# Kernel tuning notes

Hardware: AMD Instinct MI355X
Metric: run time of the kernel (lower is better)

Reference implementation:

```python
import jax, jax.numpy as jnp
import numpy as np

B, N, ND = 4096, 28, 3        # batch, nodes (2 hands x 14 joints), xyz
ED, DD = 512, 256             # encoder dim, decoder dim
H, DH = 8, 64                 # heads, dim_head (inner = 512)
EDEPTH, DDEPTH = 2, 1
EMLP, DMLP = 4 * ED, 4 * DD
NM = 14                       # num_masked = int(0.5 * 28)


def _ln(x, s, b):
    m = jnp.mean(x, -1, keepdims=True)
    v = jnp.var(x, -1, keepdims=True)
    return (x - m) * jax.lax.rsqrt(v + 1e-5) * s + b


def _transformer(x, a, ln1_s, ln1_b, Wqkv, Wo, bo, ln2_s, ln2_b, W1, b1, W2, b2):
    # pre-norm transformer; adjacency a [b,n,n] enters as an additive attention bias
    b, n, _ = x.shape
    scale = DH ** -0.5
    for i in range(ln1_s.shape[0]):
        h = _ln(x, ln1_s[i], ln1_b[i])
        q, k, v = jnp.split(h @ Wqkv[i], 3, axis=-1)
        q = q.reshape(b, n, H, DH).transpose(0, 2, 1, 3)
        k = k.reshape(b, n, H, DH).transpose(0, 2, 1, 3)
        v = v.reshape(b, n, H, DH).transpose(0, 2, 1, 3)
        dots = jnp.einsum('bhid,bhjd->bhij', q, k) * scale + a[:, None]
        attn = jax.nn.softmax(dots, axis=-1)
        o = jnp.einsum('bhij,bhjd->bhid', attn, v).transpose(0, 2, 1, 3).reshape(b, n, H * DH)
        x = x + o @ Wo[i] + bo[i]
        h2 = _ln(x, ln2_s[i], ln2_b[i])
        x = x + jax.nn.gelu(h2 @ W1[i] + b1[i]) @ W2[i] + b2[i]
    return x


def setup_inputs() -> dict:
    key = jax.random.key(0)
    ks = iter(jax.random.split(key, 40))
    nrm = lambda shp, s=0.02: jax.random.normal(next(ks), shp, dtype=jnp.float32) * s
    x = jax.random.normal(next(ks), (B, N, ND), dtype=jnp.float32)
    a = jax.random.uniform(next(ks), (B, N, N), dtype=jnp.float32)
    perm = jnp.argsort(jax.random.uniform(next(ks), (B, N)), axis=-1).astype(jnp.int32)
    masked_indices, unmasked_indices = perm[:, :NM], perm[:, NM:]
    inp = dict(x=x, a=a, masked_indices=masked_indices, unmasked_indices=unmasked_indices)
    inp.update(
        W_emb=nrm((ND, ED)), b_emb=jnp.zeros((ED,), jnp.float32), pos_emb=nrm((N, ED), 0.02),
        e_ln1_s=jnp.ones((EDEPTH, ED)), e_ln1_b=jnp.zeros((EDEPTH, ED)),
        e_Wqkv=nrm((EDEPTH, ED, 3 * H * DH)), e_Wo=nrm((EDEPTH, H * DH, ED)), e_bo=jnp.zeros((EDEPTH, ED)),
        e_ln2_s=jnp.ones((EDEPTH, ED)), e_ln2_b=jnp.zeros((EDEPTH, ED)),
        e_W1=nrm((EDEPTH, ED, EMLP)), e_b1=jnp.zeros((EDEPTH, EMLP)),
        e_W2=nrm((EDEPTH, EMLP, ED)), e_b2=jnp.zeros((EDEPTH, ED)),
        enc2dec_W=nrm((ED, DD)), enc2dec_b=jnp.zeros((DD,), jnp.float32),
        mask_token=nrm((DD,), 1.0), dec_pos_emb=nrm((N, DD), 0.02),
        d_ln1_s=jnp.ones((DDEPTH, DD)), d_ln1_b=jnp.zeros((DDEPTH, DD)),
        d_Wqkv=nrm((DDEPTH, DD, 3 * H * DH)), d_Wo=nrm((DDEPTH, H * DH, DD)), d_bo=jnp.zeros((DDEPTH, DD)),
        d_ln2_s=jnp.ones((DDEPTH, DD)), d_ln2_b=jnp.zeros((DDEPTH, DD)),
        d_W1=nrm((DDEPTH, DD, DMLP)), d_b1=jnp.zeros((DDEPTH, DMLP)),
        d_W2=nrm((DDEPTH, DMLP, DD)), d_b2=jnp.zeros((DDEPTH, DD)),
        pred_W=nrm((DD, ND)), pred_b=jnp.zeros((ND,), jnp.float32),
    )
    return inp


def reference(x, a, masked_indices, unmasked_indices,
              W_emb, b_emb, pos_emb,
              e_ln1_s, e_ln1_b, e_Wqkv, e_Wo, e_bo, e_ln2_s, e_ln2_b, e_W1, e_b1, e_W2, e_b2,
              enc2dec_W, enc2dec_b, mask_token, dec_pos_emb,
              d_ln1_s, d_ln1_b, d_Wqkv, d_Wo, d_bo, d_ln2_s, d_ln2_b, d_W1, d_b1, d_W2, d_b2,
              pred_W, pred_b):
    # node embedding (1x1 conv over nodes == per-node linear) + positional embedding
    tokens = x @ W_emb + b_emb + pos_emb                                   # [B,N,ED]
    unm_tok = jnp.take_along_axis(tokens, unmasked_indices[:, :, None], axis=1)  # [B,N-NM,ED]
    masked_nodes = jnp.take_along_axis(x, masked_indices[:, :, None], axis=1)    # [B,NM,ND]
    # batched adjacency slicing (replaces the per-sample python loop in torch)
    unmasked_a = jax.vmap(lambda ai, ii: ai[ii[:, None], ii[None, :]])(a, unmasked_indices)
    enc = _transformer(unm_tok, unmasked_a,
                       e_ln1_s, e_ln1_b, e_Wqkv, e_Wo, e_bo, e_ln2_s, e_ln2_b, e_W1, e_b1, e_W2, e_b2)
    dec_tok = enc @ enc2dec_W + enc2dec_b                                  # [B,N-NM,DD]
    mask_toks = mask_token + dec_pos_emb[masked_indices]                   # [B,NM,DD]
    # NOTE: faithful to original: unmasked pos-emb tokens are computed but NOT used in the cat
    decoder_tokens = jnp.concatenate([mask_toks, dec_tok], axis=1)         # [B,N,DD]
    decoded = _transformer(decoder_tokens, a,
                           d_ln1_s, d_ln1_b, d_Wqkv, d_Wo, d_bo, d_ln2_s, d_ln2_b, d_W1, d_b1, d_W2, d_b2)
    mt = jnp.take_along_axis(decoded, masked_indices[:, :, None], axis=1)  # [B,NM,DD]
    masked_pred = mt @ pred_W + pred_b                                     # [B,NM,ND]
    recon_loss = jnp.mean((masked_pred - masked_nodes) ** 2)
    return (decoder_tokens, masked_nodes, masked_indices, masked_pred, recon_loss)
```

## Files before the change

kernel.cpp:

```cpp
#include <hip/hip_runtime.h>
#include <math.h>

#define B_TOT 4096
#define N_SEQ 28
#define NDIM 3
#define ED 512
#define DD 256
#define NH 8
#define DHD 64
#define EMLP 2048
#define DMLP 1024
#define NM 14
#define NU 14

typedef __attribute__((ext_vector_type(8))) short short8;
typedef __attribute__((ext_vector_type(4))) float f32x4;
typedef unsigned short ushort_t;
typedef unsigned int uint_t;

__device__ __forceinline__ float gelu_f(float x) {
    float t = 0.7978845608028654f * (x + 0.044715f * x * x * x);
    float e = __expf(2.0f * t);
    float th = 1.0f - 2.0f / (e + 1.0f);
    return 0.5f * x * (1.0f + th);
}
__device__ __forceinline__ ushort_t f2bf(float f) {
    union { float f; uint_t u; } c; c.f = f;
    uint_t u = c.u;
    return (ushort_t)((u + 0x7FFFu + ((u >> 16) & 1u)) >> 16);
}
__device__ __forceinline__ float bf2f(ushort_t h) {
    union { uint_t u; float f; } c; c.u = ((uint_t)h) << 16;
    return c.f;
}
__device__ __forceinline__ float bf_lo(uint_t u) {
    union { uint_t u; float f; } c; c.u = u << 16;
    return c.f;
}
__device__ __forceinline__ float bf_hi(uint_t u) {
    union { uint_t u; float f; } c; c.u = u & 0xFFFF0000u;
    return c.f;
}
__device__ __forceinline__ void gl_lds16(const ushort_t* g, ushort_t* l) {
    __builtin_amdgcn_global_load_lds(
        (const __attribute__((address_space(1))) unsigned int*)g,
        (__attribute__((address_space(3))) unsigned int*)l, 16, 0, 0);
}

__global__ void k_zero(float* p) { p[threadIdx.x] = 0.0f; }
__global__ void k_final(const float* acc, float* out) {
    out[0] = acc[0] * (1.0f / (float)(B_TOT * NM * NDIM));
}

__global__ void k_wconv(const float* __restrict__ W, ushort_t* __restrict__ Wt, int K, int N) {
    __shared__ float tile[32][33];
    int n0 = blockIdx.x * 32, k0 = blockIdx.y * 32;
    int tr = threadIdx.x >> 5, tc = threadIdx.x & 31;
#pragma unroll
    for (int i = 0; i < 4; ++i)
        tile[tr + i * 8][tc] = W[(size_t)(k0 + tr + i * 8) * N + n0 + tc];
    __syncthreads();
#pragma unroll
    for (int i = 0; i < 4; ++i)
        Wt[(size_t)(n0 + tr + i * 8) * K + k0 + tc] = f2bf(tile[tc][tr + i * 8]);
}

__global__ void k_embed(const float* __restrict__ x, const float* __restrict__ a,
                        const int* __restrict__ mi, const int* __restrict__ ui,
                        const float* __restrict__ W_emb, const float* __restrict__ b_emb,
                        const float* __restrict__ pos_emb,
                        ushort_t* __restrict__ X, float* __restrict__ ua,
                        float* __restrict__ out_mn, float* __restrict__ out_midx,
                        int base) {
    int s = blockIdx.x;
    int g = base + s;
    int t = threadIdx.x;
    for (int i = 0; i < NU; ++i) {
        int u = ui[g * NU + i];
        float x0 = x[((size_t)g * N_SEQ + u) * NDIM + 0];
        float x1 = x[((size_t)g * N_SEQ + u) * NDIM + 1];
        float x2 = x[((size_t)g * N_SEQ + u) * NDIM + 2];
        for (int d = t; d < ED; d += 256) {
            X[((size_t)s * NU + i) * ED + d] = f2bf(
                x0 * W_emb[d] + x1 * W_emb[ED + d] + x2 * W_emb[2 * ED + d]
                + b_emb[d] + pos_emb[(size_t)u * ED + d]);
        }
    }
    for (int idx = t; idx < NU * NU; idx += 256) {
        int i = idx / NU, j = idx % NU;
        int uii = ui[g * NU + i], ujj = ui[g * NU + j];
        ua[(size_t)s * NU * NU + idx] = a[(size_t)g * N_SEQ * N_SEQ + (size_t)uii * N_SEQ + ujj];
    }
    for (int idx = t; idx < NM * NDIM; idx += 256) {
        int i = idx / NDIM, c = idx % NDIM;
        int m = mi[g * NM + i];
        out_mn[((size_t)g * NM + i) * NDIM + c] = x[((size_t)g * N_SEQ + m) * NDIM + c];
    }
    for (int i = t; i < NM; i += 256) {
        out_midx[(size_t)g * NM + i] = (float)mi[g * NM + i];
    }
}

template <int D>
__global__ void k_ln(const ushort_t* __restrict__ in, ushort_t* __restrict__ out,
                     const float* __restrict__ sc, const float* __restrict__ bi, int M) {
    int wave = threadIdx.x >> 6;
    int lane = threadIdx.x & 63;
    int row = blockIdx.x * 4 + wave;
    if (row >= M) return;
    constexpr int PL = D / 64;
    const ushort_t* rp = in + (size_t)row * D + lane * PL;
    uint_t u[PL / 2];
    if (PL == 8) *(uint4*)u = *(const uint4*)rp;
    else *(uint2*)u = *(const uint2*)rp;
    float v[PL];
    float sum = 0.f, sq = 0.f;
#pragma unroll
    for (int q = 0; q < PL / 2; ++q) {
        v[2 * q] = bf_lo(u[q]);
        v[2 * q + 1] = bf_hi(u[q]);
    }
#pragma unroll
    for (int j = 0; j < PL; ++j) { sum += v[j]; sq += v[j] * v[j]; }
#pragma unroll
    for (int o = 32; o >= 1; o >>= 1) {
        sum += __shfl_xor(sum, o);
        sq += __shfl_xor(sq, o);
    }
    float mean = sum * (1.0f / D);
    float var = sq * (1.0f / D) - mean * mean;
    float r = rsqrtf(var + 1e-5f);
    uint_t w[PL / 2];
#pragma unroll
    for (int q = 0; q < PL / 2; ++q) {
        int d = lane * PL + 2 * q;
        float a0 = (v[2 * q] - mean) * r * sc[d] + bi[d];
        float a1 = (v[2 * q + 1] - mean) * r * sc[d + 1] + bi[d + 1];
        w[q] = (uint_t)f2bf(a0) | ((uint_t)f2bf(a1) << 16);
    }
    ushort_t* op = out + (size_t)row * D + lane * PL;
    if (PL == 8) *(uint4*)op = *(uint4*)w;
    else *(uint2*)op = *(uint2*)w;
}

template <int ACT>
__global__ __launch_bounds__(256) void k_gemm_mfma(
    const ushort_t* __restrict__ A, const ushort_t* __restrict__ Wt,
    const float* __restrict__ bias, const ushort_t* __restrict__ res,
    ushort_t* __restrict__ Cout, int M, int N, int K) {
    __shared__ __align__(16) ushort_t smem[17408];
    ushort_t* As0 = smem;
    ushort_t* As1 = smem + 4096;
    ushort_t* Bs0 = smem + 8192;
    ushort_t* Bs1 = smem + 12288;

    const int t = threadIdx.x;
    const int gx = gridDim.x;
    int flat = blockIdx.y * gx + blockIdx.x;
    int nwg = gx * gridDim.y;
    int q8 = nwg >> 3, r8 = nwg & 7;
    int xcd = flat & 7, loc = flat >> 3;
    int wg = (xcd < r8 ? xcd * (q8 + 1) : r8 * (q8 + 1) + (xcd - r8) * q8) + loc;
    const int bm = wg / gx, bn = wg % gx;

    const int lane = t & 63;
    const int wave = t >> 6;
    const int wr = wave >> 1, wc = wave & 1;
    const int l15 = lane & 15;
    const int g4 = lane >> 4;
    const int kg = g4 * 8;

    const int srow = wave * 32 + (lane >> 2);
    const int scol = (lane & 3) * 8;
    const ushort_t* Ag = A + (size_t)(bm * 128 + srow) * K + scol;
    const ushort_t* Bg = Wt + (size_t)(bn * 128 + srow) * K + scol;
    const int wb0 = (wave * 32) * 32;
    const int wb1 = (wave * 32 + 16) * 32;

    f32x4 acc[4][4] = {};
    const int nt = K >> 5;

    gl_lds16(Ag, As0 + wb0);
    gl_lds16(Ag + (size_t)16 * K, As0 + wb1);
    gl_lds16(Bg, Bs0 + wb0);
    gl_lds16(Bg + (size_t)16 * K, Bs0 + wb1);

    for (int tt = 0; tt < nt; ++tt) {
        ushort_t* Ac = (tt & 1) ? As1 : As0;
        ushort_t* Bc = (tt & 1) ? Bs1 : Bs0;
        if (tt + 1 < nt) {
            int k0 = (tt + 1) << 5;
            ushort_t* An = (tt & 1) ? As0 : As1;
            ushort_t* Bn = (tt & 1) ? Bs0 : Bs1;
            gl_lds16(Ag + k0, An + wb0);
            gl_lds16(Ag + (size_t)16 * K + k0, An + wb1);
            gl_lds16(Bg + k0, Bn + wb0);
            gl_lds16(Bg + (size_t)16 * K + k0, Bn + wb1);
            asm volatile("s_waitcnt vmcnt(4)" ::: "memory");
        } else {
            asm volatile("s_waitcnt vmcnt(0)" ::: "memory");
        }
        __builtin_amdgcn_s_barrier();
        __builtin_amdgcn_sched_barrier(0);
        short8 af[4], bfr[4];
#pragma unroll
        for (int m = 0; m < 4; ++m)
            af[m] = *(const short8*)&Ac[(wr * 64 + m * 16 + l15) * 32 + kg];
#pragma unroll
        for (int n = 0; n < 4; ++n)
            bfr[n] = *(const short8*)&Bc[(wc * 64 + n * 16 + l15) * 32 + kg];
#pragma unroll
        for (int m = 0; m < 4; ++m)
#pragma unroll
            for (int n = 0; n < 4; ++n)
                acc[m][n] = __builtin_amdgcn_mfma_f32_16x16x32_bf16(af[m], bfr[n], acc[m][n], 0, 0, 0);
        __builtin_amdgcn_sched_barrier(0);
        __builtin_amdgcn_s_barrier();
    }

    ushort_t* Cs = smem;
    const int erow0 = wr * 64, ecol0 = wc * 64;
#pragma unroll
    for (int m = 0; m < 4; ++m)
#pragma unroll
        for (int n = 0; n < 4; ++n)
#pragma unroll
            for (int r = 0; r < 4; ++r) {
                float v = acc[m][n][r];
                float o = __shfl_xor(v, 1);
                if (!(l15 & 1)) {
                    uint_t pk = (uint_t)f2bf(v) | ((uint_t)f2bf(o) << 16);
                    *(uint_t*)&Cs[(erow0 + m * 16 + g4 * 4 + r) * 136 + ecol0 + n * 16 + l15] = pk;
                }
            }
    __builtin_amdgcn_s_barrier();

    const int row = t >> 1, half = t & 1;
    const int grow = bm * 128 + row;
    const int gc0 = bn * 128 + half * 64;
    const ushort_t* rres = res ? res + (size_t)grow * N + gc0 : (const ushort_t*)0;
    ushort_t* gout = Cout + (size_t)grow * N + gc0;
#pragma unroll
    for (int c = 0; c < 8; ++c) {
        uint4 pv = *(const uint4*)&Cs[row * 136 + half * 64 + c * 8];
        uint_t* pw = (uint_t*)&pv;
        float vv[8];
#pragma unroll
        for (int q = 0; q < 4; ++q) { vv[2 * q] = bf_lo(pw[q]); vv[2 * q + 1] = bf_hi(pw[q]); }
        if (bias) {
#pragma unroll
            for (int j = 0; j < 8; ++j) vv[j] += bias[gc0 + c * 8 + j];
        }
        if (res) {
            uint4 rv = *(const uint4*)(rres + c * 8);
            uint_t* pr = (uint_t*)&rv;
#pragma unroll
            for (int q = 0; q < 4; ++q) { vv[2 * q] += bf_lo(pr[q]); vv[2 * q + 1] += bf_hi(pr[q]); }
        }
        if (ACT == 1) {
#pragma unroll
            for (int j = 0; j < 8; ++j) vv[j] = gelu_f(vv[j]);
        }
        uint4 ov;
        uint_t* po = (uint_t*)&ov;
#pragma unroll
        for (int q = 0; q < 4; ++q)
            po[q] = (uint_t)f2bf(vv[2 * q]) | ((uint_t)f2bf(vv[2 * q + 1]) << 16);
        *(uint4*)(gout + c * 8) = ov;
    }
}

template <int NT>
__global__ __launch_bounds__(256) void k_attn_mfma(
    const ushort_t* __restrict__ qkv, const float* __restrict__ bias,
    ushort_t* __restrict__ O) {
    constexpr int NTP = (NT + 15) & ~15;
    constexpr int MT = NTP / 16;
    constexpr int QS = 72;
    constexpr int VS = 40;
    __shared__ __align__(16) ushort_t smem[4 * NTP * QS * 2 + 4 * 64 * VS];
    ushort_t* Qs = smem;
    ushort_t* Ks = smem + 4 * NTP * QS;
    ushort_t* Vs = Ks + 4 * NTP * QS;
    ushort_t* Ps = smem;

    const int s = blockIdx.x, hg = blockIdx.y;
    const int t = threadIdx.x;
    const int wave = t >> 6, lane = t & 63;
    const int l15 = lane & 15, g4 = lane >> 4;

    const ushort_t* qb = qkv + (size_t)s * NT * 1536 + hg * 256;
    for (int c = t; c < 64 * NT; c += 256) {
        int c8 = c & 7;
        int rem = c >> 3;
        int r = rem % NT;
        int ph = rem / NT;
        int h = ph & 3, p = ph >> 2;
        uint4 v = *(const uint4*)(qb + (size_t)r * 1536 + p * 512 + h * 64 + c8 * 8);
        ushort_t* dst = (p ? Ks : Qs) + (h * NTP + r) * QS + c8 * 8;
        *(uint4*)dst = v;
    }
    const ushort_t* vrow = qkv + (size_t)s * NT * 1536 + 1024 + hg * 256;
    for (int c = t; c < 4 * 64 * (32 - NT); c += 256) {
        int p = c % (32 - NT);
        int hd = c / (32 - NT);
        Vs[hd * VS + NT + p] = 0;
    }
    for (int c = t; c < 4 * NT * 8; c += 256) {
        int c8 = c & 7;
        int r = (c >> 3) % NT;
        int h = (c >> 3) / NT;
        uint4 v = *(const uint4*)(vrow + (size_t)r * 1536 + h * 64 + c8 * 8);
        const uint_t* pv = (const uint_t*)&v;
#pragma unroll
        for (int j = 0; j < 4; ++j) {
            Vs[(h * 64 + c8 * 8 + 2 * j) * VS + r] = (ushort_t)(pv[j] & 0xFFFFu);
            Vs[(h * 64 + c8 * 8 + 2 * j + 1) * VS + r] = (ushort_t)(pv[j] >> 16);
        }
    }
    __syncthreads();

    const int h = wave;
    const ushort_t* Qh = Qs + h * NTP * QS;
    const ushort_t* Kh = Ks + h * NTP * QS;
    const ushort_t* Vh = Vs + h * 64 * VS;
    ushort_t* Ph = Ps + h * NTP * VS;

    f32x4 sacc[MT][MT] = {};
#pragma unroll
    for (int ks = 0; ks < 2; ++ks) {
        short8 qf[MT], kf[MT];
#pragma unroll
        for (int m = 0; m < MT; ++m)
            qf[m] = *(const short8*)&Qh[(m * 16 + l15) * QS + ks * 32 + g4 * 8];
#pragma unroll
        for (int n = 0; n < MT; ++n)
            kf[n] = *(const short8*)&Kh[(n * 16 + l15) * QS + ks * 32 + g4 * 8];
#pragma unroll
        for (int m = 0; m < MT; ++m)
#pragma unroll
            for (int n = 0; n < MT; ++n)
                sacc[m][n] = __builtin_amdgcn_mfma_f32_16x16x32_bf16(qf[m], kf[n], sacc[m][n], 0, 0, 0);
    }

    const float* bp = bias + (size_t)s * NT * NT;
    float prv[MT][MT][4];
#pragma unroll
    for (int m = 0; m < MT; ++m) {
#pragma unroll
        for (int r = 0; r < 4; ++r) {
            int i = m * 16 + g4 * 4 + r;
            float sv[MT];
#pragma unroll
            for (int n = 0; n < MT; ++n) {
                int j = n * 16 + l15;
                sv[n] = (i < NT && j < NT) ? sacc[m][n][r] * 0.125f + bp[i * NT + j] : -1e30f;
            }
            float mx = sv[0];
            if (MT > 1) mx = fmaxf(mx, sv[MT - 1]);
#pragma unroll
            for (int o = 1; o < 16; o <<= 1) mx = fmaxf(mx, __shfl_xor(mx, o));
            float sum = 0.f;
#pragma unroll
            for (int n = 0; n < MT; ++n) {
                float e = (sv[n] > -1e29f) ? __expf(sv[n] - mx) : 0.f;
                prv[m][n][r] = e;
                sum += e;
            }
#pragma unroll
            for (int o = 1; o < 16; o <<= 1) sum += __shfl_xor(sum, o);
            float rs = sum > 0.f ? 1.0f / sum : 0.f;
#pragma unroll
            for (int n = 0; n < MT; ++n) prv[m][n][r] *= rs;
        }
    }
    __syncthreads();

    if (NTP == 16) {
        for (int z = lane; z < 16 * 8; z += 64) {
            int i = z >> 3, jw = z & 7;
            *(uint_t*)&Ph[i * VS + 16 + jw * 2] = 0;
        }
    }
#pragma unroll
    for (int m = 0; m < MT; ++m)
#pragma unroll
        for (int n = 0; n < MT; ++n)
#pragma unroll
            for (int r = 0; r < 4; ++r)
                Ph[(m * 16 + g4 * 4 + r) * VS + n * 16 + l15] = f2bf(prv[m][n][r]);
    __syncthreads();

    f32x4 oacc[MT][4] = {};
    {
        short8 pf[MT], vf[4];
#pragma unroll
        for (int m = 0; m < MT; ++m)
            pf[m] = *(const short8*)&Ph[(m * 16 + l15) * VS + g4 * 8];
#pragma unroll
        for (int nd = 0; nd < 4; ++nd)
            vf[nd] = *(const short8*)&Vh[(nd * 16 + l15) * VS + g4 * 8];
#pragma unroll
        for (int m = 0; m < MT; ++m)
#pragma unroll
            for (int nd = 0; nd < 4; ++nd)
                oacc[m][nd] = __builtin_amdgcn_mfma_f32_16x16x32_bf16(pf[m], vf[nd], oacc[m][nd], 0, 0, 0);
    }

    ushort_t* Ob = O + (size_t)s * NT * 512 + hg * 256 + h * 64;
#pragma unroll
    for (int m = 0; m < MT; ++m)
#pragma unroll
        for (int r = 0; r < 4; ++r) {
            int i = m * 16 + g4 * 4 + r;
            if (i < NT) {
#pragma unroll
                for (int nd = 0; nd < 4; ++nd)
                    Ob[(size_t)i * 512 + nd * 16 + l15] = f2bf(oacc[m][nd][r]);
            }
        }
}

__global__ void k_build_dec(const ushort_t* __restrict__ dec_tok, const float* __restrict__ mask_token,
                            const float* __restrict__ dec_pos, const int* __restrict__ mi,
                            ushort_t* __restrict__ Xd, float* __restrict__ out0, int base) {
    int s = blockIdx.x;
    int g = base + s;
    int t = threadIdx.x;
    for (int idx = t; idx < N_SEQ * DD; idx += 256) {
        int i = idx / DD, d = idx % DD;
        float v;
        if (i < NM) {
            int m = mi[g * NM + i];
            v = mask_token[d] + dec_pos[(size_t)m * DD + d];
        } else {
            v = bf2f(dec_tok[((size_t)s * NU + (i - NM)) * DD + d]);
        }
        Xd[((size_t)s * N_SEQ + i) * DD + d] = f2bf(v);
        out0[((size_t)g * N_SEQ + i) * DD + d] = v;
    }
}

__global__ void k_pred(const ushort_t* __restrict__ Xd, const int* __restrict__ mi,
                       const float* __restrict__ pW, const float* __restrict__ pb,
                       const float* __restrict__ mn, float* __restrict__ out_pred,
                       float* __restrict__ loss, int base, int Bc) {
    int tid = blockIdx.x * 256 + threadIdx.x;
    int total = Bc * NM * NDIM;
    float part = 0.f;
    if (tid < total) {
        int c = tid % NDIM;
        int r = tid / NDIM;
        int i = r % NM;
        int s = r / NM;
        int g = base + s;
        int m = mi[g * NM + i];
        const ushort_t* row = Xd + ((size_t)s * N_SEQ + m) * DD;
        float acc = pb[c];
        for (int k = 0; k < DD; ++k) acc += bf2f(row[k]) * pW[k * NDIM + c];
        out_pred[((size_t)g * NM + i) * NDIM + c] = acc;
        float d = acc - mn[((size_t)g * NM + i) * NDIM + c];
        part = d * d;
    }
    __shared__ float red[256];
    red[threadIdx.x] = part;
    __syncthreads();
    for (int o = 128; o > 0; o >>= 1) {
        if (threadIdx.x < o) red[threadIdx.x] += red[threadIdx.x + o];
        __syncthreads();
    }
    if (threadIdx.x == 0) atomicAdd(loss, red[0]);
}

extern "C" void kernel_launch(void* const* d_in, const int* in_sizes, int n_in,
                              void* d_out, int out_size, void* d_ws, size_t ws_size,
                              hipStream_t stream) {
    const float* x       = (const float*)d_in[0];
    const float* a       = (const float*)d_in[1];
    const int*   mi      = (const int*)d_in[2];
    const int*   ui      = (const int*)d_in[3];
    const float* W_emb   = (const float*)d_in[4];
    const float* b_emb   = (const float*)d_in[5];
    const float* pos_emb = (const float*)d_in[6];
    const float* e_ln1_s = (const float*)d_in[7];
    const float* e_ln1_b = (const float*)d_in[8];
    const float* e_Wqkv  = (const float*)d_in[9];
    const float* e_Wo    = (const float*)d_in[10];
    const float* e_bo    = (const float*)d_in[11];
    const float* e_ln2_s = (const float*)d_in[12];
    const float* e_ln2_b = (const float*)d_in[13];
    const float* e_W1    = (const float*)d_in[14];
    const float* e_b1    = (const float*)d_in[15];
    const float* e_W2    = (const float*)d_in[16];
    const float* e_b2    = (const float*)d_in[17];
    const float* e2d_W   = (const float*)d_in[18];
    const float* e2d_b   = (const float*)d_in[19];
    const float* mask_tok= (const float*)d_in[20];
    const float* dec_pos = (const float*)d_in[21];
    const float* d_ln1_s = (const float*)d_in[22];
    const float* d_ln1_b = (const float*)d_in[23];
    const float* d_Wqkv  = (const float*)d_in[24];
    const float* d_Wo    = (const float*)d_in[25];
    const float* d_bo    = (const float*)d_in[26];
    const float* d_ln2_s = (const float*)d_in[27];
    const float* d_ln2_b = (const float*)d_in[28];
    const float* d_W1    = (const float*)d_in[29];
    const float* d_b1    = (const float*)d_in[30];
    const float* d_W2    = (const float*)d_in[31];
    const float* d_b2    = (const float*)d_in[32];
    const float* pred_W  = (const float*)d_in[33];
    const float* pred_b  = (const float*)d_in[34];

    float* out0 = (float*)d_out;
    float* out1 = out0 + (size_t)B_TOT * N_SEQ * DD;
    float* out2 = out1 + (size_t)B_TOT * NM * NDIM;
    float* out3 = out2 + (size_t)B_TOT * NM;
    float* out4 = out3 + (size_t)B_TOT * NM * NDIM;

    char* wp = (char*)d_ws;
    size_t off = 0;
    auto alloc = [&](size_t bytes) {
        size_t o = off;
        off = (off + bytes + 255) & ~(size_t)255;
        return (void*)(wp + o);
    };
    float* loss_acc = (float*)alloc(64 * 4);
    ushort_t* wt_eqkv = (ushort_t*)alloc((size_t)2 * 1536 * 512 * 2);
    ushort_t* wt_ewo  = (ushort_t*)alloc((size_t)2 * 512 * 512 * 2);
    ushort_t* wt_ew1  = (ushort_t*)alloc((size_t)2 * 2048 * 512 * 2);
    ushort_t* wt_ew2  = (ushort_t*)alloc((size_t)2 * 512 * 2048 * 2);
    ushort_t* wt_dqkv = (ushort_t*)alloc((size_t)1536 * 256 * 2);
    ushort_t* wt_dwo  = (ushort_t*)alloc((size_t)256 * 512 * 2);
    ushort_t* wt_dw1  = (ushort_t*)alloc((size_t)1024 * 256 * 2);
    ushort_t* wt_dw2  = (ushort_t*)alloc((size_t)256 * 1024 * 2);
    ushort_t* wt_e2d  = (ushort_t*)alloc((size_t)256 * 512 * 2);
    size_t fixed_bytes = off;

    const size_t per_seq = 2 * (7168 + 3584 + 7168 + 43008 + 14336) + 4 * 196;
    int Bc = B_TOT;
    while (Bc > 64 && fixed_bytes + (size_t)Bc * per_seq + 8192 > ws_size) Bc >>= 1;

    ushort_t* Xbuf   = (ushort_t*)alloc((size_t)Bc * 7168 * 2);
    ushort_t* Dbuf   = (ushort_t*)alloc((size_t)Bc * 3584 * 2);
    float*    uabuf  = (float*)alloc((size_t)Bc * 196 * 4);
    ushort_t* Hbuf   = (ushort_t*)alloc((size_t)Bc * 7168 * 2);
    ushort_t* QKVbuf = (ushort_t*)alloc((size_t)Bc * 43008 * 2);
    ushort_t* Obuf   = (ushort_t*)alloc((size_t)Bc * 14336 * 2);

    k_zero<<<1, 64, 0, stream>>>(loss_acc);

    for (int l = 0; l < 2; ++l) {
        k_wconv<<<dim3(1536 / 32, 512 / 32), 256, 0, stream>>>(e_Wqkv + (size_t)l * 512 * 1536, wt_eqkv + (size_t)l * 1536 * 512, 512, 1536);
        k_wconv<<<dim3(512 / 32, 512 / 32), 256, 0, stream>>>(e_Wo + (size_t)l * 512 * 512, wt_ewo + (size_t)l * 512 * 512, 512, 512);
        k_wconv<<<dim3(2048 / 32, 512 / 32), 256, 0, stream>>>(e_W1 + (size_t)l * 512 * 2048, wt_ew1 + (size_t)l * 2048 * 512, 512, 2048);
        k_wconv<<<dim3(512 / 32, 2048 / 32), 256, 0, stream>>>(e_W2 + (size_t)l * 2048 * 512, wt_ew2 + (size_t)l * 512 * 2048, 2048, 512);
    }
    k_wconv<<<dim3(1536 / 32, 256 / 32), 256, 0, stream>>>(d_Wqkv, wt_dqkv, 256, 1536);
    k_wconv<<<dim3(256 / 32, 512 / 32), 256, 0, stream>>>(d_Wo, wt_dwo, 512, 256);
    k_wconv<<<dim3(1024 / 32, 256 / 32), 256, 0, stream>>>(d_W1, wt_dw1, 256, 1024);
    k_wconv<<<dim3(256 / 32, 1024 / 32), 256, 0, stream>>>(d_W2, wt_dw2, 1024, 256);
    k_wconv<<<dim3(256 / 32, 512 / 32), 256, 0, stream>>>(e2d_W, wt_e2d, 512, 256);

    const int nchunk = B_TOT / Bc;
    for (int c = 0; c < nchunk; ++c) {
        int base = c * Bc;
        int M = Bc * NU;
        int Md = Bc * N_SEQ;

        k_embed<<<Bc, 256, 0, stream>>>(x, a, mi, ui, W_emb, b_emb, pos_emb,
                                        Xbuf, uabuf, out1, out2, base);
        for (int l = 0; l < 2; ++l) {
            k_ln<ED><<<M / 4, 256, 0, stream>>>(Xbuf, Hbuf, e_ln1_s + l * ED, e_ln1_b + l * ED, M);
            k_gemm_mfma<0><<<dim3(1536 / 128, M / 128), 256, 0, stream>>>(
                Hbuf, wt_eqkv + (size_t)l * 1536 * 512, nullptr, nullptr, QKVbuf, M, 1536, ED);
            k_attn_mfma<NU><<<dim3(Bc, 2), 256, 0, stream>>>(QKVbuf, uabuf, Obuf);
            k_gemm_mfma<0><<<dim3(ED / 128, M / 128), 256, 0, stream>>>(
                Obuf, wt_ewo + (size_t)l * 512 * 512, e_bo + l * ED, Xbuf, Xbuf, M, ED, 512);
            k_ln<ED><<<M / 4, 256, 0, stream>>>(Xbuf, Hbuf, e_ln2_s + l * ED, e_ln2_b + l * ED, M);
            k_gemm_mfma<1><<<dim3(EMLP / 128, M / 128), 256, 0, stream>>>(
                Hbuf, wt_ew1 + (size_t)l * 2048 * 512, e_b1 + l * EMLP, nullptr, QKVbuf, M, EMLP, ED);
            k_gemm_mfma<0><<<dim3(ED / 128, M / 128), 256, 0, stream>>>(
                QKVbuf, wt_ew2 + (size_t)l * 512 * 2048, e_b2 + l * ED, Xbuf, Xbuf, M, ED, EMLP);
        }
        k_gemm_mfma<0><<<dim3(DD / 128, M / 128), 256, 0, stream>>>(
            Xbuf, wt_e2d, e2d_b, nullptr, Dbuf, M, DD, ED);
        k_build_dec<<<Bc, 256, 0, stream>>>(Dbuf, mask_tok, dec_pos, mi, Xbuf, out0, base);
        k_ln<DD><<<Md / 4, 256, 0, stream>>>(Xbuf, Hbuf, d_ln1_s, d_ln1_b, Md);
        k_gemm_mfma<0><<<dim3(1536 / 128, Md / 128), 256, 0, stream>>>(
            Hbuf, wt_dqkv, nullptr, nullptr, QKVbuf, Md, 1536, DD);
        k_attn_mfma<N_SEQ><<<dim3(Bc, 2), 256, 0, stream>>>(QKVbuf, a + (size_t)base * N_SEQ * N_SEQ, Obuf);
        k_gemm_mfma<0><<<dim3(DD / 128, Md / 128), 256, 0, stream>>>(
            Obuf, wt_dwo, d_bo, Xbuf, Xbuf, Md, DD, 512);
        k_ln<DD><<<Md / 4, 256, 0, stream>>>(Xbuf, Hbuf, d_ln2_s, d_ln2_b, Md);
        k_gemm_mfma<1><<<dim3(DMLP / 128, Md / 128), 256, 0, stream>>>(
            Hbuf, wt_dw1, d_b1, nullptr, QKVbuf, Md, DMLP, DD);
        k_gemm_mfma<0><<<dim3(DD / 128, Md / 128), 256, 0, stream>>>(
            QKVbuf, wt_dw2, d_b2, Xbuf, Xbuf, Md, DD, DMLP);
        int tot = Bc * NM * NDIM;
        k_pred<<<(tot + 255) / 256, 256, 0, stream>>>(
            Xbuf, mi, pred_W, pred_b, out1, out3, loss_acc, base, Bc);
    }
    k_final<<<1, 1, 0, stream>>>(loss_acc, out4);
}
```

Baseline: 2.845 ms.

## Load GEMM MFMA fragments directly from global memory, skipping LDS staging

The bf16 MFMA GEMM no longer copies A/B tiles into double-buffered LDS with global_load_lds and barriers. Each wave now reads its own 16-row fragments straight from global memory into registers, double-buffered over two 32-wide K steps. Launch bounds also request 3 blocks per SM. This removes LDS round-trips and workgroup barriers, but tiles shared by two waves are now fetched twice and the per-lane strided row reads lean on the L1/L2 caches for coalescing. The K loop assumes K is a multiple of 64.

```diff
diff --git a/kernel.cpp b/kernel.cpp
--- a/kernel.cpp
+++ b/kernel.cpp
@@ -40,11 +40,6 @@
 __device__ __forceinline__ float bf_hi(uint_t u) {
     union { uint_t u; float f; } c; c.u = u & 0xFFFF0000u;
     return c.f;
-}
-__device__ __forceinline__ void gl_lds16(const ushort_t* g, ushort_t* l) {
-    __builtin_amdgcn_global_load_lds(
-        (const __attribute__((address_space(1))) unsigned int*)g,
-        (__attribute__((address_space(3))) unsigned int*)l, 16, 0, 0);
 }
 
 __global__ void k_zero(float* p) { p[threadIdx.x] = 0.0f; }
@@ -143,16 +138,28 @@
     else *(uint2*)op = *(uint2*)w;
 }
 
+#define LOADF(AF, BF, KO)                                                        \
+    do {                                                                         \
+        _Pragma("unroll") for (int m_ = 0; m_ < 4; ++m_)                         \
+            AF[m_] = *(const short8*)(Aw + (size_t)m_ * 16 * K + (KO));          \
+        _Pragma("unroll") for (int n_ = 0; n_ < 4; ++n_)                         \
+            BF[n_] = *(const short8*)(Bw + (size_t)n_ * 16 * K + (KO));          \
+    } while (0)
+
+#define MFMAS(AF, BF)                                                            \
+    do {                                                                         \
+        _Pragma("unroll") for (int m_ = 0; m_ < 4; ++m_)                         \
+            _Pragma("unroll") for (int n_ = 0; n_ < 4; ++n_)                     \
+                acc[m_][n_] = __builtin_amdgcn_mfma_f32_16x16x32_bf16(           \
+                    AF[m_], BF[n_], acc[m_][n_], 0, 0, 0);                       \
+    } while (0)
+
 template <int ACT>
-__global__ __launch_bounds__(256) void k_gemm_mfma(
+__global__ __launch_bounds__(256, 3) void k_gemm_mfma(
     const ushort_t* __restrict__ A, const ushort_t* __restrict__ Wt,
     const float* __restrict__ bias, const ushort_t* __restrict__ res,
     ushort_t* __restrict__ Cout, int M, int N, int K) {
     __shared__ __align__(16) ushort_t smem[17408];
-    ushort_t* As0 = smem;
-    ushort_t* As1 = smem + 4096;
-    ushort_t* Bs0 = smem + 8192;
-    ushort_t* Bs1 = smem + 12288;
 
     const int t = threadIdx.x;
     const int gx = gridDim.x;
@@ -168,54 +175,19 @@
     const int wr = wave >> 1, wc = wave & 1;
     const int l15 = lane & 15;
     const int g4 = lane >> 4;
-    const int kg = g4 * 8;
-
-    const int srow = wave * 32 + (lane >> 2);
-    const int scol = (lane & 3) * 8;
-    const ushort_t* Ag = A + (size_t)(bm * 128 + srow) * K + scol;
-    const ushort_t* Bg = Wt + (size_t)(bn * 128 + srow) * K + scol;
-    const int wb0 = (wave * 32) * 32;
-    const int wb1 = (wave * 32 + 16) * 32;
+
+    const ushort_t* Aw = A + (size_t)(bm * 128 + wr * 64 + l15) * K + g4 * 8;
+    const ushort_t* Bw = Wt + (size_t)(bn * 128 + wc * 64 + l15) * K + g4 * 8;
 
     f32x4 acc[4][4] = {};
-    const int nt = K >> 5;
-
-    gl_lds16(Ag, As0 + wb0);
-    gl_lds16(Ag + (size_t)16 * K, As0 + wb1);
-    gl_lds16(Bg, Bs0 + wb0);
-    gl_lds16(Bg + (size_t)16 * K, Bs0 + wb1);
-
-    for (int tt = 0; tt < nt; ++tt) {
-        ushort_t* Ac = (tt & 1) ? As1 : As0;
-        ushort_t* Bc = (tt & 1) ? Bs1 : Bs0;
-        if (tt + 1 < nt) {
-            int k0 = (tt + 1) << 5;
-            ushort_t* An = (tt & 1) ? As0 : As1;
-            ushort_t* Bn = (tt & 1) ? Bs0 : Bs1;
-            gl_lds16(Ag + k0, An + wb0);
-            gl_lds16(Ag + (size_t)16 * K + k0, An + wb1);
-            gl_lds16(Bg + k0, Bn + wb0);
-            gl_lds16(Bg + (size_t)16 * K + k0, Bn + wb1);
-            asm volatile("s_waitcnt vmcnt(4)" ::: "memory");
-        } else {
-            asm volatile("s_waitcnt vmcnt(0)" ::: "memory");
-        }
-        __builtin_amdgcn_s_barrier();
-        __builtin_amdgcn_sched_barrier(0);
-        short8 af[4], bfr[4];
-#pragma unroll
-        for (int m = 0; m < 4; ++m)
-            af[m] = *(const short8*)&Ac[(wr * 64 + m * 16 + l15) * 32 + kg];
-#pragma unroll
-        for (int n = 0; n < 4; ++n)
-            bfr[n] = *(const short8*)&Bc[(wc * 64 + n * 16 + l15) * 32 + kg];
-#pragma unroll
-        for (int m = 0; m < 4; ++m)
-#pragma unroll
-            for (int n = 0; n < 4; ++n)
-                acc[m][n] = __builtin_amdgcn_mfma_f32_16x16x32_bf16(af[m], bfr[n], acc[m][n], 0, 0, 0);
-        __builtin_amdgcn_sched_barrier(0);
-        __builtin_amdgcn_s_barrier();
+    short8 a0[4], b0f[4], a1[4], b1f[4];
+
+    LOADF(a0, b0f, 0);
+    for (int k0 = 0; k0 < K; k0 += 64) {
+        if (k0 + 32 < K) LOADF(a1, b1f, k0 + 32);
+        MFMAS(a0, b0f);
+        if (k0 + 64 < K) LOADF(a0, b0f, k0 + 64);
+        MFMAS(a1, b1f);
     }
 
     ushort_t* Cs = smem;
```

Result: slower. 4.781 ms (+68.1%).
